# Performance work log

Hardware: AMD Instinct MI355X
Metric: run time of the kernel (lower is better)

## Reference

```python
import jax, jax.numpy as jnp
import numpy as np

N_GC = 8192
N_PC = 2048
PF_FANIN = 256
BATCH = 4096


def _build_mask(seed=0):
    # Matches torch logic: per Purkinje cell, pick pf_fanin random granule cells.
    rng = np.random.default_rng(seed)
    mask = np.zeros((N_PC, N_GC), dtype=np.float32)
    for p in range(N_PC):
        idx = rng.permutation(N_GC)[:PF_FANIN]
        mask[p, idx] = 1.0
    return jnp.asarray(mask)


def setup_inputs() -> dict:
    key = jax.random.key(0)
    k1, k2 = jax.random.split(key)
    g_in = jax.random.normal(k1, (BATCH, N_GC), dtype=jnp.float32)
    # kaiming_uniform-ish init for raw weights
    bound = 1.0 / np.sqrt(N_GC)
    W_raw = jax.random.uniform(k2, (N_PC, N_GC), dtype=jnp.float32, minval=-bound, maxval=bound)
    b_pc = jnp.zeros((N_PC,), dtype=jnp.float32)
    mask = _build_mask(0)
    return {"g_in": g_in, "W_raw": W_raw, "b_pc": b_pc, "mask": mask}


def reference(g_in, W_raw, b_pc, mask):
    # effective weight: softplus(W_raw) * mask, shape [n_pc, n_gc]
    W = jax.nn.softplus(W_raw) * mask
    # pc = relu(g_in @ W.T + b)  -> [batch, n_pc]
    pc = jnp.einsum('bg,pg->bp', g_in, W) + b_pc
    return jax.nn.relu(pc)
```

## Files before the change

### kernel.cpp

```cpp
#include <hip/hip_runtime.h>

#define BATCH 4096
#define NGC   8192
#define NPC   2048

typedef _Float16 f16;
typedef __attribute__((ext_vector_type(8))) _Float16 f16x8;
typedef __attribute__((ext_vector_type(4))) _Float16 f16x4;
typedef __attribute__((ext_vector_type(4))) float   floatx4;

__device__ __forceinline__ float softplus_f(float x) {
    return fmaxf(x, 0.0f) + log1pf(expf(-fabsf(x)));
}

__global__ void cvt_g(const float* __restrict__ g, f16* __restrict__ gh) {
    int i = (blockIdx.x * blockDim.x + threadIdx.x) * 4;
    float4 v = *(const float4*)(g + i);
    f16x4 h;
    h[0] = (f16)v.x; h[1] = (f16)v.y; h[2] = (f16)v.z; h[3] = (f16)v.w;
    *(f16x4*)(gh + i) = h;
}

__global__ void cvt_w(const float* __restrict__ W, const float* __restrict__ mask,
                      f16* __restrict__ wh) {
    int i = (blockIdx.x * blockDim.x + threadIdx.x) * 4;
    float4 w = *(const float4*)(W + i);
    float4 m = *(const float4*)(mask + i);
    f16x4 h;
    h[0] = (f16)(softplus_f(w.x) * m.x);
    h[1] = (f16)(softplus_f(w.y) * m.y);
    h[2] = (f16)(softplus_f(w.z) * m.z);
    h[3] = (f16)(softplus_f(w.w) * m.w);
    *(f16x4*)(wh + i) = h;
}

__device__ __forceinline__ void gload_lds16(const f16* g, f16* l) {
    __builtin_amdgcn_global_load_lds((const __attribute__((address_space(1))) void*)g,
                                     (__attribute__((address_space(3))) void*)l,
                                     16, 0, 0);
}

__global__ void gemm_f16(const f16* __restrict__ A, const f16* __restrict__ B,
                         const float* __restrict__ bias, float* __restrict__ out) {
    __shared__ __align__(16) f16 As[128 * 64];
    __shared__ __align__(16) f16 Bs[128 * 64];

    const int tid  = threadIdx.x;
    const int lane = tid & 63;
    const int wid  = tid >> 6;
    const int bm0  = blockIdx.y * 128;
    const int bn0  = blockIdx.x * 128;
    const int wm   = (wid >> 1) * 64;
    const int wn   = (wid & 1) * 64;
    const int l15  = lane & 15;
    const int lq   = lane >> 4;

    floatx4 acc[4][4] = {};

    for (int kt = 0; kt < NGC / 64; ++kt) {
        const int k0 = kt * 64;
        __syncthreads();
#pragma unroll
        for (int i = 0; i < 4; ++i) {
            int d = tid + 256 * i;
            int r = d >> 3;
            int g = (d & 7) ^ (r & 7);
            gload_lds16(A + (size_t)(bm0 + r) * NGC + k0 + g * 8, As + d * 8);
            gload_lds16(B + (size_t)(bn0 + r) * NGC + k0 + g * 8, Bs + d * 8);
        }
        __syncthreads();
#pragma unroll
        for (int ks = 0; ks < 2; ++ks) {
            const int g = ks * 4 + lq;
            f16x8 a[4], b[4];
#pragma unroll
            for (int t = 0; t < 4; ++t) {
                int ra = wm + t * 16 + l15;
                int ca = (ra << 3) | (g ^ (ra & 7));
                a[t] = *(const f16x8*)(As + ca * 8);
                int rb = wn + t * 16 + l15;
                int cb = (rb << 3) | (g ^ (rb & 7));
                b[t] = *(const f16x8*)(Bs + cb * 8);
            }
#pragma unroll
            for (int mt = 0; mt < 4; ++mt)
#pragma unroll
                for (int nt = 0; nt < 4; ++nt)
                    acc[mt][nt] = __builtin_amdgcn_mfma_f32_16x16x32_f16(
                        a[mt], b[nt], acc[mt][nt], 0, 0, 0);
        }
    }

#pragma unroll
    for (int nt = 0; nt < 4; ++nt) {
        int col  = bn0 + wn + nt * 16 + l15;
        float bv = bias[col];
#pragma unroll
        for (int mt = 0; mt < 4; ++mt) {
#pragma unroll
            for (int r = 0; r < 4; ++r) {
                int row = bm0 + wm + mt * 16 + lq * 4 + r;
                float x = acc[mt][nt][r] + bv;
                out[(size_t)row * NPC + col] = fmaxf(x, 0.0f);
            }
        }
    }
}

__global__ void naive_kernel(const float* __restrict__ g, const float* __restrict__ W,
                             const float* __restrict__ bias, const float* __restrict__ mask,
                             float* __restrict__ out) {
    int idx = blockIdx.x * 256 + threadIdx.x;
    int b = idx / NPC, p = idx % NPC;
    const float* gr = g + (size_t)b * NGC;
    const float* wr = W + (size_t)p * NGC;
    const float* mr = mask + (size_t)p * NGC;
    float acc = bias[p];
    for (int k = 0; k < NGC; ++k) {
        float m = mr[k];
        if (m != 0.0f) acc += gr[k] * softplus_f(wr[k]);
    }
    out[idx] = fmaxf(acc, 0.0f);
}

extern "C" void kernel_launch(void* const* d_in, const int* in_sizes, int n_in,
                              void* d_out, int out_size, void* d_ws, size_t ws_size,
                              hipStream_t stream) {
    const float* g_in  = (const float*)d_in[0];
    const float* W_raw = (const float*)d_in[1];
    const float* b_pc  = (const float*)d_in[2];
    const float* mask  = (const float*)d_in[3];
    float* out = (float*)d_out;

    const size_t gh_elems = (size_t)BATCH * NGC;
    const size_t wh_elems = (size_t)NPC * NGC;
    const size_t need = (gh_elems + wh_elems) * sizeof(f16);

    if (ws_size >= need) {
        f16* gh = (f16*)d_ws;
        f16* wh = gh + gh_elems;
        cvt_g<<<(int)(gh_elems / 1024), 256, 0, stream>>>(g_in, gh);
        cvt_w<<<(int)(wh_elems / 1024), 256, 0, stream>>>(W_raw, mask, wh);
        dim3 grid(NPC / 128, BATCH / 128);
        gemm_f16<<<grid, 256, 0, stream>>>(gh, wh, b_pc, out);
    } else {
        naive_kernel<<<BATCH * NPC / 256, 256, 0, stream>>>(g_in, W_raw, b_pc, mask, out);
    }
}
```

Before: 445.6 us.

## Triple-buffer LDS with async prefetch and enlarge GEMM tile to 256x128

Replaces the single-buffered load/sync/compute loop with a three-stage LDS ring. Global-to-LDS loads for tile t+2 are issued in between the MFMA groups, synchronised with vmcnt waits and a single barrier per iteration. The block tile grows to 256x128 with 512 threads (8 waves), and s_setprio is raised around the MFMA bursts. The aim is to hide global load latency and cut barrier overhead, at the cost of about 144KB of LDS per block, which limits residency.

```diff
diff --git a/kernel.cpp b/kernel.cpp
--- a/kernel.cpp
+++ b/kernel.cpp
@@ -40,15 +40,36 @@
                                      16, 0, 0);
 }
 
-__global__ void gemm_f16(const f16* __restrict__ A, const f16* __restrict__ B,
-                         const float* __restrict__ bias, float* __restrict__ out) {
-    __shared__ __align__(16) f16 As[128 * 64];
-    __shared__ __align__(16) f16 Bs[128 * 64];
+#define ABUF  (256 * 64)
+#define BBUF  (128 * 64)
+#define BUFSZ (ABUF + BBUF)
+#define NT    (NGC / 64)
+
+#define STAGE_A(kt, sbuf, i) do {                                              \
+    int d_ = tid + 512 * (i);                                                  \
+    int r_ = d_ >> 3;                                                          \
+    int g_ = (d_ & 7) ^ (r_ & 7);                                              \
+    gload_lds16(A + (size_t)(bm0 + r_) * NGC + (kt) * 64 + g_ * 8,             \
+                (sbuf) + d_ * 8);                                              \
+} while (0)
+
+#define STAGE_B(kt, sbuf, i) do {                                              \
+    int d_ = tid + 512 * (i);                                                  \
+    int r_ = d_ >> 3;                                                          \
+    int g_ = (d_ & 7) ^ (r_ & 7);                                              \
+    gload_lds16(B + (size_t)(bn0 + r_) * NGC + (kt) * 64 + g_ * 8,             \
+                (sbuf) + ABUF + d_ * 8);                                       \
+} while (0)
+
+__global__ __launch_bounds__(512, 2)
+void gemm_f16(const f16* __restrict__ A, const f16* __restrict__ B,
+              const float* __restrict__ bias, float* __restrict__ out) {
+    __shared__ __align__(16) f16 lds[3 * BUFSZ];
 
     const int tid  = threadIdx.x;
     const int lane = tid & 63;
     const int wid  = tid >> 6;
-    const int bm0  = blockIdx.y * 128;
+    const int bm0  = blockIdx.y * 256;
     const int bn0  = blockIdx.x * 128;
     const int wm   = (wid >> 1) * 64;
     const int wn   = (wid & 1) * 64;
@@ -57,38 +78,58 @@
 
     floatx4 acc[4][4] = {};
 
-    for (int kt = 0; kt < NGC / 64; ++kt) {
-        const int k0 = kt * 64;
-        __syncthreads();
 #pragma unroll
-        for (int i = 0; i < 4; ++i) {
-            int d = tid + 256 * i;
-            int r = d >> 3;
-            int g = (d & 7) ^ (r & 7);
-            gload_lds16(A + (size_t)(bm0 + r) * NGC + k0 + g * 8, As + d * 8);
-            gload_lds16(B + (size_t)(bn0 + r) * NGC + k0 + g * 8, Bs + d * 8);
-        }
-        __syncthreads();
+    for (int i = 0; i < 4; ++i) STAGE_A(0, lds, i);
+#pragma unroll
+    for (int i = 0; i < 2; ++i) STAGE_B(0, lds, i);
+#pragma unroll
+    for (int i = 0; i < 4; ++i) STAGE_A(1, lds + BUFSZ, i);
+#pragma unroll
+    for (int i = 0; i < 2; ++i) STAGE_B(1, lds + BUFSZ, i);
+
+    int cur = 0;
+    for (int t = 0; t < NT; ++t) {
+        if (t + 1 < NT) asm volatile("s_waitcnt vmcnt(6)" ::: "memory");
+        else            asm volatile("s_waitcnt vmcnt(0)" ::: "memory");
+        __builtin_amdgcn_s_barrier();
+
+        f16* sA = lds + cur * BUFSZ;
+        f16* sB = sA + ABUF;
+        int st = cur + 2; if (st >= 3) st -= 3;
+        f16* stbuf = lds + st * BUFSZ;
+        const bool do_stage = (t < NT - 2);
+
 #pragma unroll
         for (int ks = 0; ks < 2; ++ks) {
             const int g = ks * 4 + lq;
             f16x8 a[4], b[4];
 #pragma unroll
-            for (int t = 0; t < 4; ++t) {
-                int ra = wm + t * 16 + l15;
+            for (int mt = 0; mt < 4; ++mt) {
+                int ra = wm + mt * 16 + l15;
                 int ca = (ra << 3) | (g ^ (ra & 7));
-                a[t] = *(const f16x8*)(As + ca * 8);
-                int rb = wn + t * 16 + l15;
+                a[mt] = *(const f16x8*)(sA + ca * 8);
+            }
+#pragma unroll
+            for (int nt = 0; nt < 4; ++nt) {
+                int rb = wn + nt * 16 + l15;
                 int cb = (rb << 3) | (g ^ (rb & 7));
-                b[t] = *(const f16x8*)(Bs + cb * 8);
+                b[nt] = *(const f16x8*)(sB + cb * 8);
             }
+            if (do_stage) {
+                STAGE_A(t + 2, stbuf, ks * 2 + 0);
+                STAGE_A(t + 2, stbuf, ks * 2 + 1);
+                STAGE_B(t + 2, stbuf, ks);
+            }
+            __builtin_amdgcn_s_setprio(1);
 #pragma unroll
             for (int mt = 0; mt < 4; ++mt)
 #pragma unroll
                 for (int nt = 0; nt < 4; ++nt)
                     acc[mt][nt] = __builtin_amdgcn_mfma_f32_16x16x32_f16(
                         a[mt], b[nt], acc[mt][nt], 0, 0, 0);
+            __builtin_amdgcn_s_setprio(0);
         }
+        cur += 1; if (cur == 3) cur = 0;
     }
 
 #pragma unroll
@@ -141,8 +182,8 @@
         f16* wh = gh + gh_elems;
         cvt_g<<<(int)(gh_elems / 1024), 256, 0, stream>>>(g_in, gh);
         cvt_w<<<(int)(wh_elems / 1024), 256, 0, stream>>>(W_raw, mask, wh);
-        dim3 grid(NPC / 128, BATCH / 128);
-        gemm_f16<<<grid, 256, 0, stream>>>(gh, wh, b_pc, out);
+        dim3 grid(NPC / 128, BATCH / 256);
+        gemm_f16<<<grid, 512, 0, stream>>>(gh, wh, b_pc, out);
     } else {
         naive_kernel<<<BATCH * NPC / 256, 256, 0, stream>>>(g_in, W_raw, b_pc, mask, out);
     }
```

After: 410.4 us. -7.9%, faster.
